# Performance work log

Hardware: AMD Instinct MI355X
Metric: run time of the kernel (lower is better)

The kernel has to match this reference:

```python
import jax, jax.numpy as jnp
import numpy as np

B, N, DIM = 4, 4096, 512
H, DH = 8, 64
F = 256          # nb_features = min(256, int(log(4096)*32)) = 256
CS = 128         # chunk_size = min(128, n)


def setup_inputs() -> dict:
    key = jax.random.key(0)
    k1, k2, k3, k4 = jax.random.split(key, 4)
    x = jax.random.normal(k1, (B, N, DIM), jnp.float32)
    # scale linear weights like default init so activations stay well-conditioned
    w_qkv = jax.random.normal(k2, (3 * H * DH, DIM), jnp.float32) / jnp.sqrt(DIM)
    w_out = jax.random.normal(k3, (DIM, H * DH), jnp.float32) / jnp.sqrt(H * DH)
    b_out = jnp.zeros((DIM,), jnp.float32)
    # torch.qr(randn(F, DH)) -> reduced Q of shape (F, DH), orthonormal columns
    proj = jnp.linalg.qr(jax.random.normal(k4, (F, DH), jnp.float32))[0]
    return {"x": x, "w_qkv": w_qkv, "w_out": w_out, "b_out": b_out, "proj": proj}


def _kernel_fn(t, proj):
    # exp(x @ proj^T - rowmax), stabilized over the feature axis (as in source)
    tp = jnp.einsum('...d,fd->...f', t, proj)
    return jnp.exp(tp - jnp.max(tp, axis=-1, keepdims=True))


def reference(x, w_qkv, w_out, b_out, proj):
    b, n, _ = x.shape
    scale = DH ** -0.5
    c = n // CS  # number of independent local chunks

    qkv = x @ w_qkv.T                                   # [b, n, 3*h*d]
    q, k, v = jnp.split(qkv, 3, axis=-1)

    def to_chunks(t):  # [b, n, h*d] -> [b, h, c, cs, d]
        return t.reshape(b, n, H, DH).transpose(0, 2, 1, 3).reshape(b, H, c, CS, DH)

    q = to_chunks(q) * scale
    k = to_chunks(k)
    v = to_chunks(v)

    q_prime = _kernel_fn(q, proj)                       # [b, h, c, cs, f]
    k_prime = _kernel_fn(k, proj)                       # [b, h, c, cs, f]

    k_sum = k_prime.sum(axis=3)                         # [b, h, c, f]
    D = jnp.einsum('bhcsf,bhcf->bhcs', q_prime, k_sum)
    D_inv = 1.0 / (D + 0.0001)

    context = jnp.einsum('bhcsf,bhcsd->bhcfd', k_prime, v)     # [b, h, c, f, d]
    out = jnp.einsum('bhcsf,bhcfd->bhcsd', q_prime, context)   # [b, h, c, cs, d]
    out = out * D_inv[..., None]

    out = out.reshape(b, H, n, DH).transpose(0, 2, 1, 3).reshape(b, n, H * DH)
    return out @ w_out.T + b_out                        # dropout p=0 -> identity
```

## Files before the change

### kernel.cpp

```cpp
#include <hip/hip_runtime.h>

#define B_ 4
#define N_ 4096
#define DIM_ 512
#define H_ 8
#define DH_ 64
#define F_ 256
#define CS_ 128
#define M_ (B_*N_)
#define NCHUNK_ 1024

typedef __attribute__((ext_vector_type(8))) short bf16x8;
typedef __attribute__((ext_vector_type(4))) float f32x4;

__device__ __forceinline__ unsigned short f2bf(float x){
  unsigned int u = __float_as_uint(x);
  u += 0x7fffu + ((u >> 16) & 1u);
  return (unsigned short)(u >> 16);
}
__device__ __forceinline__ float bf2f(unsigned short s){
  return __uint_as_float(((unsigned int)s) << 16);
}
__device__ __forceinline__ unsigned pack2(float a, float b){
  return (unsigned)f2bf(a) | ((unsigned)f2bf(b) << 16);
}
__device__ __forceinline__ void gl2lds16(const unsigned short* g, unsigned short* l) {
  __builtin_amdgcn_global_load_lds((const __attribute__((address_space(1))) unsigned int*)g,
                                   (__attribute__((address_space(3))) unsigned int*)l,
                                   16, 0, 0);
}

__global__ __launch_bounds__(256)
void split_kernel(const float* __restrict__ src, unsigned short* __restrict__ hi,
                  unsigned short* __restrict__ lo, int n4)
{
  int idx = blockIdx.x * 256 + threadIdx.x;
  if (idx >= n4) return;
  float4 v = ((const float4*)src)[idx];
  unsigned short h0 = f2bf(v.x), h1 = f2bf(v.y), h2 = f2bf(v.z), h3 = f2bf(v.w);
  unsigned short e0 = f2bf(v.x - bf2f(h0)), e1 = f2bf(v.y - bf2f(h1));
  unsigned short e2 = f2bf(v.z - bf2f(h2)), e3 = f2bf(v.w - bf2f(h3));
  uint2 hv, lv;
  hv.x = (unsigned)h0 | ((unsigned)h1 << 16); hv.y = (unsigned)h2 | ((unsigned)h3 << 16);
  lv.x = (unsigned)e0 | ((unsigned)e1 << 16); lv.y = (unsigned)e2 | ((unsigned)e3 << 16);
  ((uint2*)hi)[idx] = hv;
  ((uint2*)lo)[idx] = lv;
}

__global__ __launch_bounds__(256)
void prep_proj(const float* __restrict__ proj, unsigned short* __restrict__ pq,
               unsigned short* __restrict__ pk)
{
  int idx = blockIdx.x * 256 + threadIdx.x;
  if (idx >= 4096) return;
  float4 v = ((const float4*)proj)[idx];
  uint2 k, q;
  k.x = pack2(v.x, v.y);           k.y = pack2(v.z, v.w);
  q.x = pack2(v.x*0.125f, v.y*0.125f); q.y = pack2(v.z*0.125f, v.w*0.125f);
  ((uint2*)pk)[idx] = k;
  ((uint2*)pq)[idx] = q;
}

template<int SPLIT, int OUT>
__global__ __launch_bounds__(256, 2)
void mfma_gemm_nt(const unsigned short* __restrict__ Ahi, const unsigned short* __restrict__ Alo,
                  const unsigned short* __restrict__ Bhi, const unsigned short* __restrict__ Blo,
                  void* __restrict__ Cm, const float* __restrict__ bias, int K, int ldc,
                  unsigned short* __restrict__ vth, unsigned short* __restrict__ vtl)
{
  __shared__ __align__(16) unsigned short sAhi[4096];
  __shared__ __align__(16) unsigned short sBhi[4096];
  __shared__ __align__(16) unsigned short sAlo[4096];
  __shared__ __align__(16) unsigned short sBlo[4096];
  const int tid = threadIdx.x, lane = tid & 63, wave = tid >> 6;
  const int bm = blockIdx.y * 128, bn = blockIdx.x * 128;
  const int srow0 = wave * 32 + (lane >> 2);
  const int srow1 = srow0 + 16;
  const int slot = lane & 3;
  const int g0 = slot ^ ((srow0 >> 1) & 3);
  const int g1 = slot ^ ((srow1 >> 1) & 3);
  const size_t aOff0 = (size_t)(bm + srow0) * K + g0 * 8;
  const size_t aOff1 = (size_t)(bm + srow1) * K + g1 * 8;
  const size_t bOff0 = (size_t)(bn + srow0) * K + g0 * 8;
  const size_t bOff1 = (size_t)(bn + srow1) * K + g1 * 8;
  const int l0 = wave * 1024, l1 = wave * 1024 + 512;
  const int fr = lane & 15, quad = lane >> 4;
  const int wr = (wave >> 1) * 64, wc = (wave & 1) * 64;
  int offA[4], offB[4];
#pragma unroll
  for (int i = 0; i < 4; ++i) {
    int ra = wr + i * 16 + fr;  offA[i] = ra * 32 + (quad ^ ((ra >> 1) & 3)) * 8;
    int rb = wc + i * 16 + fr;  offB[i] = rb * 32 + (quad ^ ((rb >> 1) & 3)) * 8;
  }
  f32x4 acc[4][4];
#pragma unroll
  for (int i = 0; i < 4; ++i)
#pragma unroll
    for (int j = 0; j < 4; ++j) acc[i][j] = {0.f, 0.f, 0.f, 0.f};

  for (int k0 = 0; k0 < K; k0 += 32) {
    gl2lds16(Ahi + aOff0 + k0, &sAhi[l0]);
    gl2lds16(Ahi + aOff1 + k0, &sAhi[l1]);
    gl2lds16(Bhi + bOff0 + k0, &sBhi[l0]);
    gl2lds16(Bhi + bOff1 + k0, &sBhi[l1]);
    if (SPLIT) {
      gl2lds16(Alo + aOff0 + k0, &sAlo[l0]);
      gl2lds16(Alo + aOff1 + k0, &sAlo[l1]);
      gl2lds16(Blo + bOff0 + k0, &sBlo[l0]);
      gl2lds16(Blo + bOff1 + k0, &sBlo[l1]);
    }
    __syncthreads();
    bf16x8 ah[4], bh[4], al[4], bl[4];
#pragma unroll
    for (int i = 0; i < 4; ++i) {
      ah[i] = *(const bf16x8*)&sAhi[offA[i]];
      bh[i] = *(const bf16x8*)&sBhi[offB[i]];
      if (SPLIT) {
        al[i] = *(const bf16x8*)&sAlo[offA[i]];
        bl[i] = *(const bf16x8*)&sBlo[offB[i]];
      }
    }
#pragma unroll
    for (int i = 0; i < 4; ++i)
#pragma unroll
      for (int j = 0; j < 4; ++j) {
        acc[i][j] = __builtin_amdgcn_mfma_f32_16x16x32_bf16(ah[i], bh[j], acc[i][j], 0, 0, 0);
        if (SPLIT) {
          acc[i][j] = __builtin_amdgcn_mfma_f32_16x16x32_bf16(ah[i], bl[j], acc[i][j], 0, 0, 0);
          acc[i][j] = __builtin_amdgcn_mfma_f32_16x16x32_bf16(al[i], bh[j], acc[i][j], 0, 0, 0);
        }
      }
    __syncthreads();
  }
#pragma unroll
  for (int j = 0; j < 4; ++j) {
    int col = bn + wc + j * 16 + fr;
    float bv = (OUT == 0 && bias) ? bias[col] : 0.f;
#pragma unroll
    for (int i = 0; i < 4; ++i) {
      int row0 = bm + wr + i * 16 + quad * 4;
      if (OUT == 0) {
        float* cp = (float*)Cm + (size_t)row0 * ldc + col;
#pragma unroll
        for (int r = 0; r < 4; ++r) cp[(size_t)r * ldc] = acc[i][j][r] + bv;
      } else if (OUT == 1) {
        unsigned short* cp = (unsigned short*)Cm + (size_t)row0 * ldc + col;
#pragma unroll
        for (int r = 0; r < 4; ++r) cp[(size_t)r * ldc] = f2bf(acc[i][j][r]);
      } else {
        int hh = col >> 6, d = col & 63;
        int bb = row0 >> 12, cc2 = (row0 >> 7) & 31, s = row0 & 127;
        int ck = bb * 256 + hh * 32 + cc2;
        size_t ad = (size_t)ck * 8192 + d * 128 + (((s >> 3) ^ (d & 15)) << 3) + (s & 7);
        float v0 = acc[i][j][0], v1 = acc[i][j][1], v2 = acc[i][j][2], v3 = acc[i][j][3];
        unsigned short h0 = f2bf(v0), h1 = f2bf(v1), h2 = f2bf(v2), h3 = f2bf(v3);
        uint2 hv, lv;
        hv.x = (unsigned)h0 | ((unsigned)h1 << 16);
        hv.y = (unsigned)h2 | ((unsigned)h3 << 16);
        lv.x = pack2(v0 - bf2f(h0), v1 - bf2f(h1));
        lv.y = pack2(v2 - bf2f(h2), v3 - bf2f(h3));
        *(uint2*)(vth + ad) = hv;
        *(uint2*)(vtl + ad) = lv;
      }
    }
  }
}

__global__ __launch_bounds__(256, 1)
void fused_chunk(const unsigned short* __restrict__ qkv_bf,
                 const unsigned short* __restrict__ projq,
                 const unsigned short* __restrict__ projk,
                 const unsigned short* __restrict__ vth_g,
                 const unsigned short* __restrict__ vtl_g,
                 unsigned short* __restrict__ attn_hi,
                 unsigned short* __restrict__ attn_lo)
{
  __shared__ __align__(16) char smem[153088];
  unsigned short* KPT = (unsigned short*)smem;
  unsigned short* QP  = (unsigned short*)(smem + 65536);
  unsigned short* X   = (unsigned short*)(smem + 131072);
  float* KS  = (float*)(smem + 147456);
  float* DI  = (float*)(smem + 148480);
  float* KSP = (float*)(smem + 148992);

  const int tid = threadIdx.x, lane = tid & 63, wave = tid >> 6;
  const int fr = lane & 15, quad = lane >> 4;
  const int chunk = blockIdx.x;
  const int b = chunk >> 8, h = (chunk >> 5) & 7, cc = chunk & 31;
  const int mbase = b * N_ + cc * CS_;

#pragma unroll
  for (int j = 0; j < 8; ++j) {
    int idx = tid + j * 256;
    int s = idx >> 4, d0 = (idx & 15) * 4;
    uint2 v = *(const uint2*)(qkv_bf + (size_t)(mbase + s) * 1024 + 512 + h * DH_ + d0);
    *(uint2*)(X + s * 64 + (((d0 >> 3) ^ (s & 7)) << 3) + (d0 & 7)) = v;
  }
  __syncthreads();

  {
    f32x4 ka[2][16];
#pragma unroll
    for (int nt = 0; nt < 16; ++nt) { ka[0][nt] = {0,0,0,0}; ka[1][nt] = {0,0,0,0}; }
#pragma unroll
    for (int ks = 0; ks < 2; ++ks) {
      bf16x8 a[2];
#pragma unroll
      for (int mt = 0; mt < 2; ++mt) {
        int s = wave * 32 + mt * 16 + fr;
        a[mt] = *(const bf16x8*)(X + s * 64 + (((ks * 4 + quad) ^ (s & 7)) << 3));
      }
#pragma unroll
      for (int nt = 0; nt < 16; ++nt) {
        bf16x8 bf = *(const bf16x8*)(projk + (size_t)(nt * 16 + fr) * 64 + ks * 32 + quad * 8);
        ka[0][nt] = __builtin_amdgcn_mfma_f32_16x16x32_bf16(a[0], bf, ka[0][nt], 0, 0, 0);
        ka[1][nt] = __builtin_amdgcn_mfma_f32_16x16x32_bf16(a[1], bf, ka[1][nt], 0, 0, 0);
      }
    }
#pragma unroll
    for (int mt = 0; mt < 2; ++mt)
#pragma unroll
      for (int r = 0; r < 4; ++r) {
        float m = ka[mt][0][r];
#pragma unroll
        for (int nt = 1; nt < 16; ++nt) m = fmaxf(m, ka[mt][nt][r]);
        m = fmaxf(m, __shfl_xor(m, 1, 16));
        m = fmaxf(m, __shfl_xor(m, 2, 16));
        m = fmaxf(m, __shfl_xor(m, 4, 16));
        m = fmaxf(m, __shfl_xor(m, 8, 16));
#pragma unroll
        for (int nt = 0; nt < 16; ++nt) ka[mt][nt][r] = __expf(ka[mt][nt][r] - m);
      }
#pragma unroll
    for (int nt = 0; nt < 16; ++nt) {
      float sm = 0.f;
#pragma unroll
      for (int mt = 0; mt < 2; ++mt)
#pragma unroll
        for (int r = 0; r < 4; ++r) sm += ka[mt][nt][r];
      sm += __shfl_xor(sm, 16, 64);
      sm += __shfl_xor(sm, 32, 64);
      if (quad == 0) KSP[wave * 256 + nt * 16 + fr] = sm;
    }
#pragma unroll
    for (int nt = 0; nt < 16; ++nt) {
      int f = nt * 16 + fr;
#pragma unroll
      for (int mt = 0; mt < 2; ++mt) {
        int g = wave * 4 + mt * 2 + (quad >> 1);
        uint2 w;
        w.x = pack2(ka[mt][nt][0], ka[mt][nt][1]);
        w.y = pack2(ka[mt][nt][2], ka[mt][nt][3]);
        *(uint2*)(KPT + f * 128 + ((g ^ (f & 15)) << 3) + (quad & 1) * 4) = w;
      }
    }
  }
  __syncthreads();

  KS[tid] = KSP[tid] + KSP[256 + tid] + KSP[512 + tid] + KSP[768 + tid];
#pragma unroll
  for (int j = 0; j < 8; ++j) {
    int idx = tid + j * 256;
    int s = idx >> 4, d0 = (idx & 15) * 4;
    uint2 v = *(const uint2*)(qkv_bf + (size_t)(mbase + s) * 1024 + h * DH_ + d0);
    *(uint2*)(X + s * 64 + (((d0 >> 3) ^ (s & 7)) << 3) + (d0 & 7)) = v;
  }
  __syncthreads();

  {
    f32x4 qa[16][2];
#pragma unroll
    for (int mt = 0; mt < 16; ++mt) { qa[mt][0] = {0,0,0,0}; qa[mt][1] = {0,0,0,0}; }
#pragma unroll
    for (int ks = 0; ks < 2; ++ks) {
      bf16x8 bfr[2];
#pragma unroll
      for (int nt = 0; nt < 2; ++nt) {
        int s = wave * 32 + nt * 16 + fr;
        bfr[nt] = *(const bf16x8*)(X + s * 64 + (((ks * 4 + quad) ^ (s & 7)) << 3));
      }
#pragma unroll
      for (int mt = 0; mt < 16; ++mt) {
        bf16x8 af = *(const bf16x8*)(projq + (size_t)(mt * 16 + fr) * 64 + ks * 32 + quad * 8);
        qa[mt][0] = __builtin_amdgcn_mfma_f32_16x16x32_bf16(af, bfr[0], qa[mt][0], 0, 0, 0);
        qa[mt][1] = __builtin_amdgcn_mfma_f32_16x16x32_bf16(af, bfr[1], qa[mt][1], 0, 0, 0);
      }
    }
#pragma unroll
    for (int nt = 0; nt < 2; ++nt) {
      float m = -1e30f;
#pragma unroll
      for (int mt = 0; mt < 16; ++mt)
#pragma unroll
        for (int r = 0; r < 4; ++r) m = fmaxf(m, qa[mt][nt][r]);
      m = fmaxf(m, __shfl_xor(m, 16, 64));
      m = fmaxf(m, __shfl_xor(m, 32, 64));
#pragma unroll
      for (int mt = 0; mt < 16; ++mt)
#pragma unroll
        for (int r = 0; r < 4; ++r) qa[mt][nt][r] = __expf(qa[mt][nt][r] - m);
    }
#pragma unroll
    for (int nt = 0; nt < 2; ++nt) {
      int s = wave * 32 + nt * 16 + fr;
#pragma unroll
      for (int mt = 0; mt < 16; ++mt) {
        int g = mt * 2 + (quad >> 1);
        uint2 w;
        w.x = pack2(qa[mt][nt][0], qa[mt][nt][1]);
        w.y = pack2(qa[mt][nt][2], qa[mt][nt][3]);
        *(uint2*)(QP + s * 256 + ((g ^ (s & 15)) << 3) + (quad & 1) * 4) = w;
      }
    }
  }
  __syncthreads();

  const unsigned short* vhs = vth_g + (size_t)chunk * 8192;
  const unsigned short* vls = vtl_g + (size_t)chunk * 8192;
#pragma unroll
  for (int i = 0; i < 4; ++i) gl2lds16(vhs + (wave*4+i)*512 + lane*8, X + (wave*4+i)*512);
  __syncthreads();

  f32x4 acc_a[4][4];
#pragma unroll
  for (int i = 0; i < 4; ++i)
#pragma unroll
    for (int j = 0; j < 4; ++j) acc_a[i][j] = {0.f, 0.f, 0.f, 0.f};
#pragma unroll
  for (int ks = 0; ks < 4; ++ks) {
    int l = ks * 4 + quad;
    bf16x8 a[4];
#pragma unroll
    for (int mt = 0; mt < 4; ++mt) {
      int f = wave * 64 + mt * 16 + fr;
      a[mt] = *(const bf16x8*)(KPT + f * 128 + ((l ^ (f & 15)) << 3));
    }
#pragma unroll
    for (int nt = 0; nt < 4; ++nt) {
      int d = nt * 16 + fr;
      bf16x8 bh = *(const bf16x8*)(X + d * 128 + ((l ^ (d & 15)) << 3));
#pragma unroll
      for (int mt = 0; mt < 4; ++mt)
        acc_a[mt][nt] = __builtin_amdgcn_mfma_f32_16x16x32_bf16(a[mt], bh, acc_a[mt][nt], 0, 0, 0);
    }
  }
  __syncthreads();
#pragma unroll
  for (int i = 0; i < 4; ++i) gl2lds16(vls + (wave*4+i)*512 + lane*8, X + (wave*4+i)*512);
  __syncthreads();
#pragma unroll
  for (int ks = 0; ks < 4; ++ks) {
    int l = ks * 4 + quad;
    bf16x8 a[4];
#pragma unroll
    for (int mt = 0; mt < 4; ++mt) {
      int f = wave * 64 + mt * 16 + fr;
      a[mt] = *(const bf16x8*)(KPT + f * 128 + ((l ^ (f & 15)) << 3));
    }
#pragma unroll
    for (int nt = 0; nt < 4; ++nt) {
      int d = nt * 16 + fr;
      bf16x8 bl = *(const bf16x8*)(X + d * 128 + ((l ^ (d & 15)) << 3));
#pragma unroll
      for (int mt = 0; mt < 4; ++mt)
        acc_a[mt][nt] = __builtin_amdgcn_mfma_f32_16x16x32_bf16(a[mt], bl, acc_a[mt][nt], 0, 0, 0);
    }
  }
  __syncthreads();

#pragma unroll
  for (int mt = 0; mt < 4; ++mt)
#pragma unroll
    for (int nt = 0; nt < 4; ++nt) {
      int f0 = wave * 64 + mt * 16 + quad * 4;
      int d = nt * 16 + fr;
      int g = wave * 8 + mt * 2 + (quad >> 1);
      float v0 = acc_a[mt][nt][0], v1 = acc_a[mt][nt][1];
      float v2 = acc_a[mt][nt][2], v3 = acc_a[mt][nt][3];
      unsigned short h0 = f2bf(v0), h1 = f2bf(v1), h2 = f2bf(v2), h3 = f2bf(v3);
      uint2 whi, wlo;
      whi.x = (unsigned)h0 | ((unsigned)h1 << 16);
      whi.y = (unsigned)h2 | ((unsigned)h3 << 16);
      wlo.x = pack2(v0 - bf2f(h0), v1 - bf2f(h1));
      wlo.y = pack2(v2 - bf2f(h2), v3 - bf2f(h3));
      int ad = d * 256 + ((g ^ (d & 15)) << 3) + (quad & 1) * 4;
      *(uint2*)(KPT + ad) = whi;
      *(uint2*)(KPT + 16384 + ad) = wlo;
      (void)f0;
    }
  __syncthreads();

  if (tid < 128) {
    int s = tid;
    float dp = 0.f;
#pragma unroll 4
    for (int l = 0; l < 32; ++l) {
      bf16x8 qv = *(const bf16x8*)(QP + s * 256 + ((l ^ (s & 15)) << 3));
      f32x4 k0 = *(const f32x4*)(KS + l * 8);
      f32x4 k1 = *(const f32x4*)(KS + l * 8 + 4);
      dp += bf2f((unsigned short)qv[0]) * k0[0];
      dp += bf2f((unsigned short)qv[1]) * k0[1];
      dp += bf2f((unsigned short)qv[2]) * k0[2];
      dp += bf2f((unsigned short)qv[3]) * k0[3];
      dp += bf2f((unsigned short)qv[4]) * k1[0];
      dp += bf2f((unsigned short)qv[5]) * k1[1];
      dp += bf2f((unsigned short)qv[6]) * k1[2];
      dp += bf2f((unsigned short)qv[7]) * k1[3];
    }
    DI[s] = 1.f / (dp + 1e-4f);
  }
  __syncthreads();

  f32x4 acc2[4][2];
#pragma unroll
  for (int i = 0; i < 4; ++i) { acc2[i][0] = {0,0,0,0}; acc2[i][1] = {0,0,0,0}; }
#pragma unroll
  for (int ks = 0; ks < 8; ++ks) {
    int l = ks * 4 + quad;
    bf16x8 ah[4], al[4];
#pragma unroll
    for (int mt = 0; mt < 4; ++mt) {
      int d = mt * 16 + fr;
      int ad = d * 256 + ((l ^ (d & 15)) << 3);
      ah[mt] = *(const bf16x8*)(KPT + ad);
      al[mt] = *(const bf16x8*)(KPT + 16384 + ad);
    }
#pragma unroll
    for (int nt = 0; nt < 2; ++nt) {
      int s = wave * 32 + nt * 16 + fr;
      bf16x8 bq = *(const bf16x8*)(QP + s * 256 + ((l ^ (s & 15)) << 3));
#pragma unroll
      for (int mt = 0; mt < 4; ++mt) {
        acc2[mt][nt] = __builtin_amdgcn_mfma_f32_16x16x32_bf16(ah[mt], bq, acc2[mt][nt], 0, 0, 0);
        acc2[mt][nt] = __builtin_amdgcn_mfma_f32_16x16x32_bf16(al[mt], bq, acc2[mt][nt], 0, 0, 0);
      }
    }
  }
#pragma unroll
  for (int nt = 0; nt < 2; ++nt) {
    int s = wave * 32 + nt * 16 + fr;
    float di = DI[s];
    size_t base = (size_t)(mbase + s) * 512 + h * DH_;
#pragma unroll
    for (int mt = 0; mt < 4; ++mt) {
      int d0 = mt * 16 + quad * 4;
      float o0 = acc2[mt][nt][0] * di, o1 = acc2[mt][nt][1] * di;
      float o2 = acc2[mt][nt][2] * di, o3 = acc2[mt][nt][3] * di;
      unsigned short h0 = f2bf(o0), h1 = f2bf(o1), h2 = f2bf(o2), h3 = f2bf(o3);
      uint2 whi, wlo;
      whi.x = (unsigned)h0 | ((unsigned)h1 << 16);
      whi.y = (unsigned)h2 | ((unsigned)h3 << 16);
      wlo.x = pack2(o0 - bf2f(h0), o1 - bf2f(h1));
      wlo.y = pack2(o2 - bf2f(h2), o3 - bf2f(h3));
      *(uint2*)(attn_hi + base + d0) = whi;
      *(uint2*)(attn_lo + base + d0) = wlo;
    }
  }
}

extern "C" void kernel_launch(void* const* d_in, const int* in_sizes, int n_in,
                              void* d_out, int out_size, void* d_ws, size_t ws_size,
                              hipStream_t stream)
{
  const float* x     = (const float*)d_in[0];
  const float* w_qkv = (const float*)d_in[1];
  const float* w_out = (const float*)d_in[2];
  const float* b_out = (const float*)d_in[3];
  const float* proj  = (const float*)d_in[4];
  float* out = (float*)d_out;

  char* ws = (char*)d_ws;
  unsigned short* qkv_bf = (unsigned short*)ws;
  unsigned short* x_hi   = (unsigned short*)(ws + 33554432);
  unsigned short* x_lo   = x_hi + (size_t)M_ * DIM_;
  unsigned short* wqkv_hi = (unsigned short*)(ws + 67108864);
  unsigned short* wqkv_lo = wqkv_hi + (size_t)(3*DIM_) * DIM_;
  unsigned short* attn_hi = (unsigned short*)(ws + 134217728);
  unsigned short* attn_lo = attn_hi + (size_t)M_ * DIM_;
  unsigned short* vth_g  = (unsigned short*)(ws + 201326592);
  unsigned short* vtl_g  = (unsigned short*)(ws + 218103808);

  unsigned short* projq = x_hi;
  unsigned short* projk = projq + 16384;
  unsigned short* wout_hi = projk + 16384;
  unsigned short* wout_lo = wout_hi + (size_t)DIM_ * DIM_;

  split_kernel<<<dim3(M_*DIM_/4/256), 256, 0, stream>>>(x, x_hi, x_lo, M_*DIM_/4);
  split_kernel<<<dim3(3*DIM_*DIM_/4/256), 256, 0, stream>>>(w_qkv, wqkv_hi, wqkv_lo, 3*DIM_*DIM_/4);
  mfma_gemm_nt<0,1><<<dim3(8, M_/128), 256, 0, stream>>>(
      x_hi, x_hi, wqkv_hi, wqkv_hi, qkv_bf, nullptr, DIM_, 1024, nullptr, nullptr);
  mfma_gemm_nt<1,2><<<dim3(4, M_/128), 256, 0, stream>>>(
      x_hi, x_lo, wqkv_hi + (size_t)1024*DIM_, wqkv_lo + (size_t)1024*DIM_,
      nullptr, nullptr, DIM_, 0, vth_g, vtl_g);
  prep_proj<<<dim3(16), 256, 0, stream>>>(proj, projq, projk);
  fused_chunk<<<dim3(NCHUNK_), 256, 0, stream>>>(qkv_bf, projq, projk, vth_g, vtl_g,
                                                 attn_hi, attn_lo);
  split_kernel<<<dim3(DIM_*DIM_/4/256), 256, 0, stream>>>(w_out, wout_hi, wout_lo, DIM_*DIM_/4);
  mfma_gemm_nt<1,0><<<dim3(4, M_/128), 256, 0, stream>>>(
      attn_hi, attn_lo, wout_hi, wout_lo, out, b_out, DIM_, DIM_, nullptr, nullptr);
}
```

Measured before the change: 281.7 us.

## Use 512 threads per block in fused chunk kernel to halve per-wave work

Doubles the block size of the fused per-chunk attention kernel from 4 to 8 waves, redistributing every stage (K/Q feature maps, context GEMM, denominator, output GEMM) so each wave handles half as many rows. The LDS partial-sum buffer grows to hold 8 wave partials, and the denominator dot product is split across two halves with an extra reduction step. The aim is more latency hiding and MFMA parallelism per CU, since only one block fits per CU because of the large LDS footprint. In exchange, each wave reuses loaded operands less, and the kernel adds barriers plus a small extra reduction.

New measurement: 297.9 us. 5.8% more time.

```diff
diff --git a/kernel.cpp b/kernel.cpp
--- a/kernel.cpp
+++ b/kernel.cpp
@@ -166,7 +166,7 @@
   }
 }
 
-__global__ __launch_bounds__(256, 1)
+__global__ __launch_bounds__(512, 1)
 void fused_chunk(const unsigned short* __restrict__ qkv_bf,
                  const unsigned short* __restrict__ projq,
                  const unsigned short* __restrict__ projk,
@@ -175,7 +175,7 @@
                  unsigned short* __restrict__ attn_hi,
                  unsigned short* __restrict__ attn_lo)
 {
-  __shared__ __align__(16) char smem[153088];
+  __shared__ __align__(16) char smem[157184];
   unsigned short* KPT = (unsigned short*)smem;
   unsigned short* QP  = (unsigned short*)(smem + 65536);
   unsigned short* X   = (unsigned short*)(smem + 131072);
@@ -190,8 +190,8 @@
   const int mbase = b * N_ + cc * CS_;
 
 #pragma unroll
-  for (int j = 0; j < 8; ++j) {
-    int idx = tid + j * 256;
+  for (int j = 0; j < 4; ++j) {
+    int idx = tid + j * 512;
     int s = idx >> 4, d0 = (idx & 15) * 4;
     uint2 v = *(const uint2*)(qkv_bf + (size_t)(mbase + s) * 1024 + 512 + h * DH_ + d0);
     *(uint2*)(X + s * 64 + (((d0 >> 3) ^ (s & 7)) << 3) + (d0 & 7)) = v;
@@ -199,68 +199,58 @@
   __syncthreads();
 
   {
-    f32x4 ka[2][16];
-#pragma unroll
-    for (int nt = 0; nt < 16; ++nt) { ka[0][nt] = {0,0,0,0}; ka[1][nt] = {0,0,0,0}; }
+    f32x4 ka[16];
+#pragma unroll
+    for (int nt = 0; nt < 16; ++nt) ka[nt] = {0.f, 0.f, 0.f, 0.f};
 #pragma unroll
     for (int ks = 0; ks < 2; ++ks) {
-      bf16x8 a[2];
-#pragma unroll
-      for (int mt = 0; mt < 2; ++mt) {
-        int s = wave * 32 + mt * 16 + fr;
-        a[mt] = *(const bf16x8*)(X + s * 64 + (((ks * 4 + quad) ^ (s & 7)) << 3));
-      }
+      int s = wave * 16 + fr;
+      bf16x8 a = *(const bf16x8*)(X + s * 64 + (((ks * 4 + quad) ^ (s & 7)) << 3));
 #pragma unroll
       for (int nt = 0; nt < 16; ++nt) {
         bf16x8 bf = *(const bf16x8*)(projk + (size_t)(nt * 16 + fr) * 64 + ks * 32 + quad * 8);
-        ka[0][nt] = __builtin_amdgcn_mfma_f32_16x16x32_bf16(a[0], bf, ka[0][nt], 0, 0, 0);
-        ka[1][nt] = __builtin_amdgcn_mfma_f32_16x16x32_bf16(a[1], bf, ka[1][nt], 0, 0, 0);
+        ka[nt] = __builtin_amdgcn_mfma_f32_16x16x32_bf16(a, bf, ka[nt], 0, 0, 0);
       }
     }
 #pragma unroll
-    for (int mt = 0; mt < 2; ++mt)
-#pragma unroll
-      for (int r = 0; r < 4; ++r) {
-        float m = ka[mt][0][r];
-#pragma unroll
-        for (int nt = 1; nt < 16; ++nt) m = fmaxf(m, ka[mt][nt][r]);
-        m = fmaxf(m, __shfl_xor(m, 1, 16));
-        m = fmaxf(m, __shfl_xor(m, 2, 16));
-        m = fmaxf(m, __shfl_xor(m, 4, 16));
-        m = fmaxf(m, __shfl_xor(m, 8, 16));
-#pragma unroll
-        for (int nt = 0; nt < 16; ++nt) ka[mt][nt][r] = __expf(ka[mt][nt][r] - m);
-      }
+    for (int r = 0; r < 4; ++r) {
+      float m = ka[0][r];
+#pragma unroll
+      for (int nt = 1; nt < 16; ++nt) m = fmaxf(m, ka[nt][r]);
+      m = fmaxf(m, __shfl_xor(m, 1, 16));
+      m = fmaxf(m, __shfl_xor(m, 2, 16));
+      m = fmaxf(m, __shfl_xor(m, 4, 16));
+      m = fmaxf(m, __shfl_xor(m, 8, 16));
+#pragma unroll
+      for (int nt = 0; nt < 16; ++nt) ka[nt][r] = __expf(ka[nt][r] - m);
+    }
 #pragma unroll
     for (int nt = 0; nt < 16; ++nt) {
-      float sm = 0.f;
-#pragma unroll
-      for (int mt = 0; mt < 2; ++mt)
-#pragma unroll
-        for (int r = 0; r < 4; ++r) sm += ka[mt][nt][r];
+      float sm = ka[nt][0] + ka[nt][1] + ka[nt][2] + ka[nt][3];
       sm += __shfl_xor(sm, 16, 64);
       sm += __shfl_xor(sm, 32, 64);
       if (quad == 0) KSP[wave * 256 + nt * 16 + fr] = sm;
     }
+    const int g = wave * 2 + (quad >> 1);
 #pragma unroll
     for (int nt = 0; nt < 16; ++nt) {
       int f = nt * 16 + fr;
-#pragma unroll
-      for (int mt = 0; mt < 2; ++mt) {
-        int g = wave * 4 + mt * 2 + (quad >> 1);
-        uint2 w;
-        w.x = pack2(ka[mt][nt][0], ka[mt][nt][1]);
-        w.y = pack2(ka[mt][nt][2], ka[mt][nt][3]);
-        *(uint2*)(KPT + f * 128 + ((g ^ (f & 15)) << 3) + (quad & 1) * 4) = w;
-      }
-    }
-  }
-  __syncthreads();
-
-  KS[tid] = KSP[tid] + KSP[256 + tid] + KSP[512 + tid] + KSP[768 + tid];
-#pragma unroll
-  for (int j = 0; j < 8; ++j) {
-    int idx = tid + j * 256;
+      uint2 w;
+      w.x = pack2(ka[nt][0], ka[nt][1]);
+      w.y = pack2(ka[nt][2], ka[nt][3]);
+      *(uint2*)(KPT + f * 128 + ((g ^ (f & 15)) << 3) + (quad & 1) * 4) = w;
+    }
+  }
+  __syncthreads();
+
+  if (tid < 256) {
+    float s0 = KSP[tid]       + KSP[256 + tid]  + KSP[512 + tid]  + KSP[768 + tid];
+    float s1 = KSP[1024 + tid] + KSP[1280 + tid] + KSP[1536 + tid] + KSP[1792 + tid];
+    KS[tid] = s0 + s1;
+  }
+#pragma unroll
+  for (int j = 0; j < 4; ++j) {
+    int idx = tid + j * 512;
     int s = idx >> 4, d0 = (idx & 15) * 4;
     uint2 v = *(const uint2*)(qkv_bf + (size_t)(mbase + s) * 1024 + h * DH_ + d0);
     *(uint2*)(X + s * 64 + (((d0 >> 3) ^ (s & 7)) << 3) + (d0 & 7)) = v;
@@ -268,49 +258,40 @@
   __syncthreads();
 
   {
-    f32x4 qa[16][2];
-#pragma unroll
-    for (int mt = 0; mt < 16; ++mt) { qa[mt][0] = {0,0,0,0}; qa[mt][1] = {0,0,0,0}; }
+    f32x4 qa[16];
+#pragma unroll
+    for (int mt = 0; mt < 16; ++mt) qa[mt] = {0.f, 0.f, 0.f, 0.f};
 #pragma unroll
     for (int ks = 0; ks < 2; ++ks) {
-      bf16x8 bfr[2];
-#pragma unroll
-      for (int nt = 0; nt < 2; ++nt) {
-        int s = wave * 32 + nt * 16 + fr;
-        bfr[nt] = *(const bf16x8*)(X + s * 64 + (((ks * 4 + quad) ^ (s & 7)) << 3));
-      }
+      int s = wave * 16 + fr;
+      bf16x8 bfr = *(const bf16x8*)(X + s * 64 + (((ks * 4 + quad) ^ (s & 7)) << 3));
 #pragma unroll
       for (int mt = 0; mt < 16; ++mt) {
         bf16x8 af = *(const bf16x8*)(projq + (size_t)(mt * 16 + fr) * 64 + ks * 32 + quad * 8);
-        qa[mt][0] = __builtin_amdgcn_mfma_f32_16x16x32_bf16(af, bfr[0], qa[mt][0], 0, 0, 0);
-        qa[mt][1] = __builtin_amdgcn_mfma_f32_16x16x32_bf16(af, bfr[1], qa[mt][1], 0, 0, 0);
+        qa[mt] = __builtin_amdgcn_mfma_f32_16x16x32_bf16(af, bfr, qa[mt], 0, 0, 0);
       }
     }
-#pragma unroll
-    for (int nt = 0; nt < 2; ++nt) {
+    {
       float m = -1e30f;
 #pragma unroll
       for (int mt = 0; mt < 16; ++mt)
 #pragma unroll
-        for (int r = 0; r < 4; ++r) m = fmaxf(m, qa[mt][nt][r]);
+        for (int r = 0; r < 4; ++r) m = fmaxf(m, qa[mt][r]);
       m = fmaxf(m, __shfl_xor(m, 16, 64));
       m = fmaxf(m, __shfl_xor(m, 32, 64));
 #pragma unroll
       for (int mt = 0; mt < 16; ++mt)
 #pragma unroll
-        for (int r = 0; r < 4; ++r) qa[mt][nt][r] = __expf(qa[mt][nt][r] - m);
-    }
-#pragma unroll
-    for (int nt = 0; nt < 2; ++nt) {
-      int s = wave * 32 + nt * 16 + fr;
-#pragma unroll
-      for (int mt = 0; mt < 16; ++mt) {
-        int g = mt * 2 + (quad >> 1);
-        uint2 w;
-        w.x = pack2(qa[mt][nt][0], qa[mt][nt][1]);
-        w.y = pack2(qa[mt][nt][2], qa[mt][nt][3]);
-        *(uint2*)(QP + s * 256 + ((g ^ (s & 15)) << 3) + (quad & 1) * 4) = w;
-      }
+        for (int r = 0; r < 4; ++r) qa[mt][r] = __expf(qa[mt][r] - m);
+    }
+    const int s = wave * 16 + fr;
+#pragma unroll
+    for (int mt = 0; mt < 16; ++mt) {
+      int g = mt * 2 + (quad >> 1);
+      uint2 w;
+      w.x = pack2(qa[mt][0], qa[mt][1]);
+      w.y = pack2(qa[mt][2], qa[mt][3]);
+      *(uint2*)(QP + s * 256 + ((g ^ (s & 15)) << 3) + (quad & 1) * 4) = w;
     }
   }
   __syncthreads();
@@ -318,21 +299,21 @@
   const unsigned short* vhs = vth_g + (size_t)chunk * 8192;
   const unsigned short* vls = vtl_g + (size_t)chunk * 8192;
 #pragma unroll
-  for (int i = 0; i < 4; ++i) gl2lds16(vhs + (wave*4+i)*512 + lane*8, X + (wave*4+i)*512);
-  __syncthreads();
-
-  f32x4 acc_a[4][4];
-#pragma unroll
-  for (int i = 0; i < 4; ++i)
+  for (int i = 0; i < 2; ++i) gl2lds16(vhs + (wave*2+i)*512 + lane*8, X + (wave*2+i)*512);
+  __syncthreads();
+
+  f32x4 acc_a[2][4];
+#pragma unroll
+  for (int i = 0; i < 2; ++i)
 #pragma unroll
     for (int j = 0; j < 4; ++j) acc_a[i][j] = {0.f, 0.f, 0.f, 0.f};
 #pragma unroll
   for (int ks = 0; ks < 4; ++ks) {
     int l = ks * 4 + quad;
-    bf16x8 a[4];
-#pragma unroll
-    for (int mt = 0; mt < 4; ++mt) {
-      int f = wave * 64 + mt * 16 + fr;
+    bf16x8 a[2];
+#pragma unroll
+    for (int mt = 0; mt < 2; ++mt) {
+      int f = wave * 32 + mt * 16 + fr;
       a[mt] = *(const bf16x8*)(KPT + f * 128 + ((l ^ (f & 15)) << 3));
     }
 #pragma unroll
@@ -340,21 +321,21 @@
       int d = nt * 16 + fr;
       bf16x8 bh = *(const bf16x8*)(X + d * 128 + ((l ^ (d & 15)) << 3));
 #pragma unroll
-      for (int mt = 0; mt < 4; ++mt)
+      for (int mt = 0; mt < 2; ++mt)
         acc_a[mt][nt] = __builtin_amdgcn_mfma_f32_16x16x32_bf16(a[mt], bh, acc_a[mt][nt], 0, 0, 0);
     }
   }
   __syncthreads();
 #pragma unroll
-  for (int i = 0; i < 4; ++i) gl2lds16(vls + (wave*4+i)*512 + lane*8, X + (wave*4+i)*512);
+  for (int i = 0; i < 2; ++i) gl2lds16(vls + (wave*2+i)*512 + lane*8, X + (wave*2+i)*512);
   __syncthreads();
 #pragma unroll
   for (int ks = 0; ks < 4; ++ks) {
     int l = ks * 4 + quad;
-    bf16x8 a[4];
-#pragma unroll
-    for (int mt = 0; mt < 4; ++mt) {
-      int f = wave * 64 + mt * 16 + fr;
+    bf16x8 a[2];
+#pragma unroll
+    for (int mt = 0; mt < 2; ++mt) {
+      int f = wave * 32 + mt * 16 + fr;
       a[mt] = *(const bf16x8*)(KPT + f * 128 + ((l ^ (f & 15)) << 3));
     }
 #pragma unroll
@@ -362,19 +343,18 @@
       int d = nt * 16 + fr;
       bf16x8 bl = *(const bf16x8*)(X + d * 128 + ((l ^ (d & 15)) << 3));
 #pragma unroll
-      for (int mt = 0; mt < 4; ++mt)
+      for (int mt = 0; mt < 2; ++mt)
         acc_a[mt][nt] = __builtin_amdgcn_mfma_f32_16x16x32_bf16(a[mt], bl, acc_a[mt][nt], 0, 0, 0);
     }
   }
   __syncthreads();
 
 #pragma unroll
-  for (int mt = 0; mt < 4; ++mt)
+  for (int mt = 0; mt < 2; ++mt)
 #pragma unroll
     for (int nt = 0; nt < 4; ++nt) {
-      int f0 = wave * 64 + mt * 16 + quad * 4;
       int d = nt * 16 + fr;
-      int g = wave * 8 + mt * 2 + (quad >> 1);
+      int g = wave * 4 + mt * 2 + (quad >> 1);
       float v0 = acc_a[mt][nt][0], v1 = acc_a[mt][nt][1];
       float v2 = acc_a[mt][nt][2], v3 = acc_a[mt][nt][3];
       unsigned short h0 = f2bf(v0), h1 = f2bf(v1), h2 = f2bf(v2), h3 = f2bf(v3);
@@ -386,15 +366,16 @@
       int ad = d * 256 + ((g ^ (d & 15)) << 3) + (quad & 1) * 4;
       *(uint2*)(KPT + ad) = whi;
       *(uint2*)(KPT + 16384 + ad) = wlo;
-      (void)f0;
-    }
-  __syncthreads();
-
-  if (tid < 128) {
-    int s = tid;
+    }
+  __syncthreads();
+
+  float* DP = KSP;
+  if (tid < 256) {
+    int s = tid & 127, hf = tid >> 7;
     float dp = 0.f;
 #pragma unroll 4
-    for (int l = 0; l < 32; ++l) {
+    for (int li = 0; li < 16; ++li) {
+      int l = hf * 16 + li;
       bf16x8 qv = *(const bf16x8*)(QP + s * 256 + ((l ^ (s & 15)) << 3));
       f32x4 k0 = *(const f32x4*)(KS + l * 8);
       f32x4 k1 = *(const f32x4*)(KS + l * 8 + 4);
@@ -407,45 +388,39 @@
       dp += bf2f((unsigned short)qv[6]) * k1[2];
       dp += bf2f((unsigned short)qv[7]) * k1[3];
     }
-    DI[s] = 1.f / (dp + 1e-4f);
-  }
-  __syncthreads();
-
-  f32x4 acc2[4][2];
-#pragma unroll
-  for (int i = 0; i < 4; ++i) { acc2[i][0] = {0,0,0,0}; acc2[i][1] = {0,0,0,0}; }
+    DP[hf * 128 + s] = dp;
+  }
+  __syncthreads();
+  if (tid < 128) DI[tid] = 1.f / (DP[tid] + DP[128 + tid] + 1e-4f);
+  __syncthreads();
+
+  f32x4 acc2[4];
+#pragma unroll
+  for (int i = 0; i < 4; ++i) acc2[i] = {0.f, 0.f, 0.f, 0.f};
 #pragma unroll
   for (int ks = 0; ks < 8; ++ks) {
     int l = ks * 4 + quad;
-    bf16x8 ah[4], al[4];
+    int s = wave * 16 + fr;
+    bf16x8 bq = *(const bf16x8*)(QP + s * 256 + ((l ^ (s & 15)) << 3));
 #pragma unroll
     for (int mt = 0; mt < 4; ++mt) {
       int d = mt * 16 + fr;
       int ad = d * 256 + ((l ^ (d & 15)) << 3);
-      ah[mt] = *(const bf16x8*)(KPT + ad);
-      al[mt] = *(const bf16x8*)(KPT + 16384 + ad);
-    }
-#pragma unroll
-    for (int nt = 0; nt < 2; ++nt) {
-      int s = wave * 32 + nt * 16 + fr;
-      bf16x8 bq = *(const bf16x8*)(QP + s * 256 + ((l ^ (s & 15)) << 3));
-#pragma unroll
-      for (int mt = 0; mt < 4; ++mt) {
-        acc2[mt][nt] = __builtin_amdgcn_mfma_f32_16x16x32_bf16(ah[mt], bq, acc2[mt][nt], 0, 0, 0);
-        acc2[mt][nt] = __builtin_amdgcn_mfma_f32_16x16x32_bf16(al[mt], bq, acc2[mt][nt], 0, 0, 0);
-      }
-    }
-  }
-#pragma unroll
-  for (int nt = 0; nt < 2; ++nt) {
-    int s = wave * 32 + nt * 16 + fr;
+      bf16x8 ah = *(const bf16x8*)(KPT + ad);
+      bf16x8 al = *(const bf16x8*)(KPT + 16384 + ad);
+      acc2[mt] = __builtin_amdgcn_mfma_f32_16x16x32_bf16(ah, bq, acc2[mt], 0, 0, 0);
+      acc2[mt] = __builtin_amdgcn_mfma_f32_16x16x32_bf16(al, bq, acc2[mt], 0, 0, 0);
+    }
+  }
+  {
+    int s = wave * 16 + fr;
     float di = DI[s];
     size_t base = (size_t)(mbase + s) * 512 + h * DH_;
 #pragma unroll
     for (int mt = 0; mt < 4; ++mt) {
       int d0 = mt * 16 + quad * 4;
-      float o0 = acc2[mt][nt][0] * di, o1 = acc2[mt][nt][1] * di;
-      float o2 = acc2[mt][nt][2] * di, o3 = acc2[mt][nt][3] * di;
+      float o0 = acc2[mt][0] * di, o1 = acc2[mt][1] * di;
+      float o2 = acc2[mt][2] * di, o3 = acc2[mt][3] * di;
       unsigned short h0 = f2bf(o0), h1 = f2bf(o1), h2 = f2bf(o2), h3 = f2bf(o3);
       uint2 whi, wlo;
       whi.x = (unsigned)h0 | ((unsigned)h1 << 16);
@@ -493,7 +468,7 @@
       x_hi, x_lo, wqkv_hi + (size_t)1024*DIM_, wqkv_lo + (size_t)1024*DIM_,
       nullptr, nullptr, DIM_, 0, vth_g, vtl_g);
   prep_proj<<<dim3(16), 256, 0, stream>>>(proj, projq, projk);
-  fused_chunk<<<dim3(NCHUNK_), 256, 0, stream>>>(qkv_bf, projq, projk, vth_g, vtl_g,
+  fused_chunk<<<dim3(NCHUNK_), 512, 0, stream>>>(qkv_bf, projq, projk, vth_g, vtl_g,
                                                  attn_hi, attn_lo);
   split_kernel<<<dim3(DIM_*DIM_/4/256), 256, 0, stream>>>(w_out, wout_hi, wout_lo, DIM_*DIM_/4);
   mfma_gemm_nt<1,0><<<dim3(4, M_/128), 256, 0, stream>>>(
```

## Split fused chunk kernel into two kernels to halve LDS and double occupancy

Applied to the files above, without the earlier changes.

The single per-chunk kernel that used about 150KB of LDS is split in two. chunkA computes k' features, the k-sum and the context matrix, then writes the context as hi/lo bf16 plus the k-sum to global workspace. chunkB computes q', the denominator and the output from that workspace. Each kernel uses about 68-80KB of LDS with launch_bounds(256,2), so two blocks can share a CU. Q and K tiles are now loaded straight into registers instead of staged through LDS. The cost is an extra launch and a global write and read of the context, 64MB hi+lo.

Measured after the change: 297.6 us. 5.7% more time.

```diff
diff --git a/kernel.cpp b/kernel.cpp
--- a/kernel.cpp
+++ b/kernel.cpp
@@ -166,57 +166,47 @@
   }
 }
 
-__global__ __launch_bounds__(256, 1)
-void fused_chunk(const unsigned short* __restrict__ qkv_bf,
-                 const unsigned short* __restrict__ projq,
-                 const unsigned short* __restrict__ projk,
-                 const unsigned short* __restrict__ vth_g,
-                 const unsigned short* __restrict__ vtl_g,
-                 unsigned short* __restrict__ attn_hi,
-                 unsigned short* __restrict__ attn_lo)
+__global__ __launch_bounds__(256, 2)
+void chunkA(const unsigned short* __restrict__ qkv_bf,
+            const unsigned short* __restrict__ projk,
+            const unsigned short* __restrict__ vth_g,
+            const unsigned short* __restrict__ vtl_g,
+            unsigned short* __restrict__ ctxh_g,
+            unsigned short* __restrict__ ctxl_g,
+            float* __restrict__ ksum_g)
 {
-  __shared__ __align__(16) char smem[153088];
+  __shared__ __align__(16) char smem[81920];
   unsigned short* KPT = (unsigned short*)smem;
-  unsigned short* QP  = (unsigned short*)(smem + 65536);
-  unsigned short* X   = (unsigned short*)(smem + 131072);
-  float* KS  = (float*)(smem + 147456);
-  float* DI  = (float*)(smem + 148480);
-  float* KSP = (float*)(smem + 148992);
+  unsigned short* X   = (unsigned short*)(smem + 65536);
+  float* KSP = (float*)(smem + 65536);
 
   const int tid = threadIdx.x, lane = tid & 63, wave = tid >> 6;
   const int fr = lane & 15, quad = lane >> 4;
   const int chunk = blockIdx.x;
   const int b = chunk >> 8, h = (chunk >> 5) & 7, cc = chunk & 31;
   const int mbase = b * N_ + cc * CS_;
-
-#pragma unroll
-  for (int j = 0; j < 8; ++j) {
-    int idx = tid + j * 256;
-    int s = idx >> 4, d0 = (idx & 15) * 4;
-    uint2 v = *(const uint2*)(qkv_bf + (size_t)(mbase + s) * 1024 + 512 + h * DH_ + d0);
-    *(uint2*)(X + s * 64 + (((d0 >> 3) ^ (s & 7)) << 3) + (d0 & 7)) = v;
-  }
-  __syncthreads();
+  const unsigned short* tkbase = qkv_bf + (size_t)mbase * 1024 + 512 + h * DH_;
 
   {
+    bf16x8 a[2][2];
+#pragma unroll
+    for (int mt = 0; mt < 2; ++mt)
+#pragma unroll
+      for (int ks = 0; ks < 2; ++ks) {
+        int s = wave * 32 + mt * 16 + fr;
+        a[mt][ks] = *(const bf16x8*)(tkbase + (size_t)s * 1024 + ks * 32 + quad * 8);
+      }
     f32x4 ka[2][16];
 #pragma unroll
     for (int nt = 0; nt < 16; ++nt) { ka[0][nt] = {0,0,0,0}; ka[1][nt] = {0,0,0,0}; }
 #pragma unroll
-    for (int ks = 0; ks < 2; ++ks) {
-      bf16x8 a[2];
-#pragma unroll
-      for (int mt = 0; mt < 2; ++mt) {
-        int s = wave * 32 + mt * 16 + fr;
-        a[mt] = *(const bf16x8*)(X + s * 64 + (((ks * 4 + quad) ^ (s & 7)) << 3));
-      }
+    for (int ks = 0; ks < 2; ++ks)
 #pragma unroll
       for (int nt = 0; nt < 16; ++nt) {
         bf16x8 bf = *(const bf16x8*)(projk + (size_t)(nt * 16 + fr) * 64 + ks * 32 + quad * 8);
-        ka[0][nt] = __builtin_amdgcn_mfma_f32_16x16x32_bf16(a[0], bf, ka[0][nt], 0, 0, 0);
-        ka[1][nt] = __builtin_amdgcn_mfma_f32_16x16x32_bf16(a[1], bf, ka[1][nt], 0, 0, 0);
-      }
-    }
+        ka[0][nt] = __builtin_amdgcn_mfma_f32_16x16x32_bf16(a[0][ks], bf, ka[0][nt], 0, 0, 0);
+        ka[1][nt] = __builtin_amdgcn_mfma_f32_16x16x32_bf16(a[1][ks], bf, ka[1][nt], 0, 0, 0);
+      }
 #pragma unroll
     for (int mt = 0; mt < 2; ++mt)
 #pragma unroll
@@ -256,63 +246,8 @@
     }
   }
   __syncthreads();
-
-  KS[tid] = KSP[tid] + KSP[256 + tid] + KSP[512 + tid] + KSP[768 + tid];
-#pragma unroll
-  for (int j = 0; j < 8; ++j) {
-    int idx = tid + j * 256;
-    int s = idx >> 4, d0 = (idx & 15) * 4;
-    uint2 v = *(const uint2*)(qkv_bf + (size_t)(mbase + s) * 1024 + h * DH_ + d0);
-    *(uint2*)(X + s * 64 + (((d0 >> 3) ^ (s & 7)) << 3) + (d0 & 7)) = v;
-  }
-  __syncthreads();
-
-  {
-    f32x4 qa[16][2];
-#pragma unroll
-    for (int mt = 0; mt < 16; ++mt) { qa[mt][0] = {0,0,0,0}; qa[mt][1] = {0,0,0,0}; }
-#pragma unroll
-    for (int ks = 0; ks < 2; ++ks) {
-      bf16x8 bfr[2];
-#pragma unroll
-      for (int nt = 0; nt < 2; ++nt) {
-        int s = wave * 32 + nt * 16 + fr;
-        bfr[nt] = *(const bf16x8*)(X + s * 64 + (((ks * 4 + quad) ^ (s & 7)) << 3));
-      }
-#pragma unroll
-      for (int mt = 0; mt < 16; ++mt) {
-        bf16x8 af = *(const bf16x8*)(projq + (size_t)(mt * 16 + fr) * 64 + ks * 32 + quad * 8);
-        qa[mt][0] = __builtin_amdgcn_mfma_f32_16x16x32_bf16(af, bfr[0], qa[mt][0], 0, 0, 0);
-        qa[mt][1] = __builtin_amdgcn_mfma_f32_16x16x32_bf16(af, bfr[1], qa[mt][1], 0, 0, 0);
-      }
-    }
-#pragma unroll
-    for (int nt = 0; nt < 2; ++nt) {
-      float m = -1e30f;
-#pragma unroll
-      for (int mt = 0; mt < 16; ++mt)
-#pragma unroll
-        for (int r = 0; r < 4; ++r) m = fmaxf(m, qa[mt][nt][r]);
-      m = fmaxf(m, __shfl_xor(m, 16, 64));
-      m = fmaxf(m, __shfl_xor(m, 32, 64));
-#pragma unroll
-      for (int mt = 0; mt < 16; ++mt)
-#pragma unroll
-        for (int r = 0; r < 4; ++r) qa[mt][nt][r] = __expf(qa[mt][nt][r] - m);
-    }
-#pragma unroll
-    for (int nt = 0; nt < 2; ++nt) {
-      int s = wave * 32 + nt * 16 + fr;
-#pragma unroll
-      for (int mt = 0; mt < 16; ++mt) {
-        int g = mt * 2 + (quad >> 1);
-        uint2 w;
-        w.x = pack2(qa[mt][nt][0], qa[mt][nt][1]);
-        w.y = pack2(qa[mt][nt][2], qa[mt][nt][3]);
-        *(uint2*)(QP + s * 256 + ((g ^ (s & 15)) << 3) + (quad & 1) * 4) = w;
-      }
-    }
-  }
+  ksum_g[(size_t)chunk * 256 + tid] =
+      KSP[tid] + KSP[256 + tid] + KSP[512 + tid] + KSP[768 + tid];
   __syncthreads();
 
   const unsigned short* vhs = vth_g + (size_t)chunk * 8192;
@@ -366,15 +301,15 @@
         acc_a[mt][nt] = __builtin_amdgcn_mfma_f32_16x16x32_bf16(a[mt], bl, acc_a[mt][nt], 0, 0, 0);
     }
   }
-  __syncthreads();
-
+
+  unsigned short* ch = ctxh_g + (size_t)chunk * 16384;
+  unsigned short* cl = ctxl_g + (size_t)chunk * 16384;
 #pragma unroll
   for (int mt = 0; mt < 4; ++mt)
 #pragma unroll
     for (int nt = 0; nt < 4; ++nt) {
       int f0 = wave * 64 + mt * 16 + quad * 4;
       int d = nt * 16 + fr;
-      int g = wave * 8 + mt * 2 + (quad >> 1);
       float v0 = acc_a[mt][nt][0], v1 = acc_a[mt][nt][1];
       float v2 = acc_a[mt][nt][2], v3 = acc_a[mt][nt][3];
       unsigned short h0 = f2bf(v0), h1 = f2bf(v1), h2 = f2bf(v2), h3 = f2bf(v3);
@@ -383,18 +318,90 @@
       whi.y = (unsigned)h2 | ((unsigned)h3 << 16);
       wlo.x = pack2(v0 - bf2f(h0), v1 - bf2f(h1));
       wlo.y = pack2(v2 - bf2f(h2), v3 - bf2f(h3));
-      int ad = d * 256 + ((g ^ (d & 15)) << 3) + (quad & 1) * 4;
-      *(uint2*)(KPT + ad) = whi;
-      *(uint2*)(KPT + 16384 + ad) = wlo;
-      (void)f0;
-    }
-  __syncthreads();
-
-  if (tid < 128) {
-    int s = tid;
+      *(uint2*)(ch + d * 256 + f0) = whi;
+      *(uint2*)(cl + d * 256 + f0) = wlo;
+    }
+}
+
+__global__ __launch_bounds__(256, 2)
+void chunkB(const unsigned short* __restrict__ qkv_bf,
+            const unsigned short* __restrict__ projq,
+            const unsigned short* __restrict__ ctxh_g,
+            const unsigned short* __restrict__ ctxl_g,
+            const float* __restrict__ ksum_g,
+            unsigned short* __restrict__ attn_hi,
+            unsigned short* __restrict__ attn_lo)
+{
+  __shared__ __align__(16) char smem[68096];
+  unsigned short* QP = (unsigned short*)smem;
+  float* KS = (float*)(smem + 65536);
+  float* DP = (float*)(smem + 66560);
+  float* DI = (float*)(smem + 67584);
+
+  const int tid = threadIdx.x, lane = tid & 63, wave = tid >> 6;
+  const int fr = lane & 15, quad = lane >> 4;
+  const int chunk = blockIdx.x;
+  const int b = chunk >> 8, h = (chunk >> 5) & 7, cc = chunk & 31;
+  const int mbase = b * N_ + cc * CS_;
+  const unsigned short* tqbase = qkv_bf + (size_t)mbase * 1024 + h * DH_;
+
+  KS[tid] = ksum_g[(size_t)chunk * 256 + tid];
+
+  {
+    bf16x8 bfr[2][2];
+#pragma unroll
+    for (int nt = 0; nt < 2; ++nt)
+#pragma unroll
+      for (int ks = 0; ks < 2; ++ks) {
+        int s = wave * 32 + nt * 16 + fr;
+        bfr[nt][ks] = *(const bf16x8*)(tqbase + (size_t)s * 1024 + ks * 32 + quad * 8);
+      }
+    f32x4 qa[16][2];
+#pragma unroll
+    for (int mt = 0; mt < 16; ++mt) { qa[mt][0] = {0,0,0,0}; qa[mt][1] = {0,0,0,0}; }
+#pragma unroll
+    for (int ks = 0; ks < 2; ++ks)
+#pragma unroll
+      for (int mt = 0; mt < 16; ++mt) {
+        bf16x8 af = *(const bf16x8*)(projq + (size_t)(mt * 16 + fr) * 64 + ks * 32 + quad * 8);
+        qa[mt][0] = __builtin_amdgcn_mfma_f32_16x16x32_bf16(af, bfr[0][ks], qa[mt][0], 0, 0, 0);
+        qa[mt][1] = __builtin_amdgcn_mfma_f32_16x16x32_bf16(af, bfr[1][ks], qa[mt][1], 0, 0, 0);
+      }
+#pragma unroll
+    for (int nt = 0; nt < 2; ++nt) {
+      float m = -1e30f;
+#pragma unroll
+      for (int mt = 0; mt < 16; ++mt)
+#pragma unroll
+        for (int r = 0; r < 4; ++r) m = fmaxf(m, qa[mt][nt][r]);
+      m = fmaxf(m, __shfl_xor(m, 16, 64));
+      m = fmaxf(m, __shfl_xor(m, 32, 64));
+#pragma unroll
+      for (int mt = 0; mt < 16; ++mt)
+#pragma unroll
+        for (int r = 0; r < 4; ++r) qa[mt][nt][r] = __expf(qa[mt][nt][r] - m);
+    }
+#pragma unroll
+    for (int nt = 0; nt < 2; ++nt) {
+      int s = wave * 32 + nt * 16 + fr;
+#pragma unroll
+      for (int mt = 0; mt < 16; ++mt) {
+        int g = mt * 2 + (quad >> 1);
+        uint2 w;
+        w.x = pack2(qa[mt][nt][0], qa[mt][nt][1]);
+        w.y = pack2(qa[mt][nt][2], qa[mt][nt][3]);
+        *(uint2*)(QP + s * 256 + ((g ^ (s & 15)) << 3) + (quad & 1) * 4) = w;
+      }
+    }
+  }
+  __syncthreads();
+
+  {
+    int s = tid & 127, hf = tid >> 7;
     float dp = 0.f;
 #pragma unroll 4
-    for (int l = 0; l < 32; ++l) {
+    for (int li = 0; li < 16; ++li) {
+      int l = hf * 16 + li;
       bf16x8 qv = *(const bf16x8*)(QP + s * 256 + ((l ^ (s & 15)) << 3));
       f32x4 k0 = *(const f32x4*)(KS + l * 8);
       f32x4 k1 = *(const f32x4*)(KS + l * 8 + 4);
@@ -407,10 +414,14 @@
       dp += bf2f((unsigned short)qv[6]) * k1[2];
       dp += bf2f((unsigned short)qv[7]) * k1[3];
     }
-    DI[s] = 1.f / (dp + 1e-4f);
-  }
-  __syncthreads();
-
+    DP[hf * 128 + s] = dp;
+  }
+  __syncthreads();
+  if (tid < 128) DI[tid] = 1.f / (DP[tid] + DP[128 + tid] + 1e-4f);
+  __syncthreads();
+
+  const unsigned short* ch = ctxh_g + (size_t)chunk * 16384;
+  const unsigned short* cl = ctxl_g + (size_t)chunk * 16384;
   f32x4 acc2[4][2];
 #pragma unroll
   for (int i = 0; i < 4; ++i) { acc2[i][0] = {0,0,0,0}; acc2[i][1] = {0,0,0,0}; }
@@ -421,9 +432,9 @@
 #pragma unroll
     for (int mt = 0; mt < 4; ++mt) {
       int d = mt * 16 + fr;
-      int ad = d * 256 + ((l ^ (d & 15)) << 3);
-      ah[mt] = *(const bf16x8*)(KPT + ad);
-      al[mt] = *(const bf16x8*)(KPT + 16384 + ad);
+      int off = d * 256 + ks * 32 + quad * 8;
+      ah[mt] = *(const bf16x8*)(ch + off);
+      al[mt] = *(const bf16x8*)(cl + off);
     }
 #pragma unroll
     for (int nt = 0; nt < 2; ++nt) {
@@ -475,10 +486,13 @@
   unsigned short* x_lo   = x_hi + (size_t)M_ * DIM_;
   unsigned short* wqkv_hi = (unsigned short*)(ws + 67108864);
   unsigned short* wqkv_lo = wqkv_hi + (size_t)(3*DIM_) * DIM_;
+  unsigned short* ctxh_g  = (unsigned short*)(ws + 67108864);
+  unsigned short* ctxl_g  = (unsigned short*)(ws + 100663296);
   unsigned short* attn_hi = (unsigned short*)(ws + 134217728);
   unsigned short* attn_lo = attn_hi + (size_t)M_ * DIM_;
   unsigned short* vth_g  = (unsigned short*)(ws + 201326592);
   unsigned short* vtl_g  = (unsigned short*)(ws + 218103808);
+  float*          ksum_g = (float*)(ws + 234881024);
 
   unsigned short* projq = x_hi;
   unsigned short* projk = projq + 16384;
@@ -493,8 +507,10 @@
       x_hi, x_lo, wqkv_hi + (size_t)1024*DIM_, wqkv_lo + (size_t)1024*DIM_,
       nullptr, nullptr, DIM_, 0, vth_g, vtl_g);
   prep_proj<<<dim3(16), 256, 0, stream>>>(proj, projq, projk);
-  fused_chunk<<<dim3(NCHUNK_), 256, 0, stream>>>(qkv_bf, projq, projk, vth_g, vtl_g,
-                                                 attn_hi, attn_lo);
+  chunkA<<<dim3(NCHUNK_), 256, 0, stream>>>(qkv_bf, projk, vth_g, vtl_g,
+                                            ctxh_g, ctxl_g, ksum_g);
+  chunkB<<<dim3(NCHUNK_), 256, 0, stream>>>(qkv_bf, projq, ctxh_g, ctxl_g, ksum_g,
+                                            attn_hi, attn_lo);
   split_kernel<<<dim3(DIM_*DIM_/4/256), 256, 0, stream>>>(w_out, wout_hi, wout_lo, DIM_*DIM_/4);
   mfma_gemm_nt<1,0><<<dim3(4, M_/128), 256, 0, stream>>>(
       attn_hi, attn_lo, wout_hi, wout_lo, out, b_out, DIM_, DIM_, nullptr, nullptr);
```
